# Optimization experiments

Measured on AMD Instinct MI355X. Metric: run time of the kernel, lower is better.

Reference implementation:

```python
import jax, jax.numpy as jnp
import numpy as np

B = 64          # batch
N_IN = 1_000_000  # SNPs (n_inputs)
N_OUT = 20_000    # genes (n_outputs = mask.shape[1])
KMAX = 64         # filter_size = max SNPs per gene


def setup_inputs() -> dict:
    key = jax.random.key(0)
    k1, k2, k3, k4 = jax.random.split(key, 4)
    x = jax.random.normal(k1, (B, N_IN), dtype=jnp.float32)
    kernel = jax.random.normal(k2, (KMAX, N_OUT), dtype=jnp.float32) * 0.05
    bias = jnp.zeros((N_OUT, 1), dtype=jnp.float32)
    # static COO mask encoded as padded per-gene index table + valid lengths
    gather_idx = jax.random.randint(k3, (N_OUT, KMAX), 0, N_IN, dtype=jnp.int32)
    lengths = jax.random.randint(k4, (N_OUT,), 1, KMAX + 1, dtype=jnp.int32)
    return {"x": x, "kernel": kernel, "bias": bias,
            "gather_idx": gather_idx, "lengths": lengths}


def reference(x, kernel, bias, gather_idx, lengths):
    # valid[g,k] = 1 if slot k of gene g holds a real SNP (padding mask)
    valid = (jnp.arange(KMAX, dtype=lengths.dtype)[None, :] < lengths[:, None])
    # per-gene weights, zeroed at padded slots: (G, K)
    w = jnp.where(valid, kernel.T, jnp.zeros((), dtype=kernel.dtype))
    # gather inputs per gene group: (B, G, K)
    gathered = x[:, gather_idx]
    # grouped multiply-reduce: (B, G)
    out = jnp.einsum('bgk,gk->bg', gathered, w)
    # bias per (gene, filter), filters = 1 -> output (B, G, 1)
    out = out[..., None] + bias[None, :, :]
    return out  # linear activation
```

## Files before the change

### kernel.cpp

```cpp
#include <hip/hip_runtime.h>
#include <hip/hip_bf16.h>

#define B_DIM 64
#define N_IN 1000000
#define N_OUT 20000
#define KMAX 64
#define GPB 16

__device__ __forceinline__ unsigned short f32_to_bf16_bits(float f) {
    __hip_bfloat16 b = __float2bfloat16(f);
    unsigned short s;
    __builtin_memcpy(&s, &b, sizeof(s));
    return s;
}

#define ZERO_BLOCKS 245
__global__ __launch_bounds__(256) void prep_kernel(
    uint4* __restrict__ flags4, const float* __restrict__ kern, float* __restrict__ wT) {
    if (blockIdx.x < ZERO_BLOCKS) {
        int tid = blockIdx.x * 256 + threadIdx.x;
        if (tid < N_IN / 16) flags4[tid] = uint4{0, 0, 0, 0};
        return;
    }
    __shared__ float lds[64 * 65];
    const int c0 = (blockIdx.x - ZERO_BLOCKS) * 64;
    const int t  = threadIdx.x;
    const int cq = t & 63;
    const int rq = t >> 6;
#pragma unroll
    for (int i = 0; i < 16; ++i) {
        int r = i * 4 + rq;
        int c = c0 + cq;
        if (c < N_OUT) lds[r * 65 + cq] = kern[r * N_OUT + c];
    }
    __syncthreads();
#pragma unroll
    for (int i = 0; i < 16; ++i) {
        int c = i * 4 + rq;
        int r = cq;
        if (c0 + c < N_OUT) wT[(c0 + c) * 64 + r] = lds[r * 65 + c];
    }
}

__global__ __launch_bounds__(256) void build_flags(
    const int* __restrict__ gidx, const int* __restrict__ lengths,
    unsigned char* __restrict__ flags) {
    int tid = blockIdx.x * 256 + threadIdx.x;
    int g = tid >> 6, k = tid & 63;
    if (g < N_OUT && k < lengths[g]) flags[gidx[g * KMAX + k]] = 1;
    if (tid == 0) flags[0] = 1;
}

__global__ __launch_bounds__(256) void transpose_x_bf16_masked(
    const float* __restrict__ src, __hip_bfloat16* __restrict__ dst,
    const unsigned char* __restrict__ flags) {
    __shared__ float ldsT[64 * 65];
    __shared__ unsigned char f[64];
    const int t  = threadIdx.x;
    const int c0 = blockIdx.x * 64;
    if (t < 64) f[t] = flags[c0 + t];
    const int col4 = (t & 15) * 4;
    const int r0   = t >> 4;
#pragma unroll
    for (int i = 0; i < 4; ++i) {
        int r = r0 + 16 * i;
        float4 v = *reinterpret_cast<const float4*>(&src[(size_t)r * N_IN + c0 + col4]);
        ldsT[(col4 + 0) * 65 + r] = v.x;
        ldsT[(col4 + 1) * 65 + r] = v.y;
        ldsT[(col4 + 2) * 65 + r] = v.z;
        ldsT[(col4 + 3) * 65 + r] = v.w;
    }
    __syncthreads();
    const int m = t & 15;
    const int cb = t >> 4;
#pragma unroll
    for (int i = 0; i < 4; ++i) {
        int c = cb + 16 * i;
        if (f[c]) {
            ushort4 h;
            h.x = f32_to_bf16_bits(ldsT[c * 65 + m * 4 + 0]);
            h.y = f32_to_bf16_bits(ldsT[c * 65 + m * 4 + 1]);
            h.z = f32_to_bf16_bits(ldsT[c * 65 + m * 4 + 2]);
            h.w = f32_to_bf16_bits(ldsT[c * 65 + m * 4 + 3]);
            *reinterpret_cast<ushort4*>(&dst[(size_t)(c0 + c) * 64 + m * 4]) = h;
        }
    }
}

__global__ __launch_bounds__(1024) void gather_dot_fused(
    const __hip_bfloat16* __restrict__ xT,
    const float* __restrict__ wT,
    const int*   __restrict__ gidx,
    const int*   __restrict__ lengths,
    const float* __restrict__ bias,
    float*       __restrict__ out) {
    __shared__ float sm[64 * 17];
    const int wave = threadIdx.x >> 6;
    const int lane = threadIdx.x & 63;
    const int half = lane >> 5;
    const int l    = lane & 31;
    const int g0   = blockIdx.x * GPB;
    const int g    = g0 + wave;

    const int len = lengths[g];
    const int   idx_l = (lane < len) ? gidx[g * KMAX + lane] : 0;
    const float w_l   = (lane < len) ? wT[g * KMAX + lane] : 0.0f;

    float acc0 = 0.0f, acc1 = 0.0f;
    for (int k = 0; k < len; k += 8) {
#pragma unroll
        for (int j = 0; j < 4; ++j) {
            int   kk  = k + 2 * j + half;
            int   row = __shfl(idx_l, kk);
            float w   = __shfl(w_l, kk);
            unsigned int u = *reinterpret_cast<const unsigned int*>(
                &xT[(size_t)row * 64 + 2 * l]);
            float f0 = __uint_as_float(u << 16);
            float f1 = __uint_as_float(u & 0xFFFF0000u);
            acc0 = fmaf(f0, w, acc0);
            acc1 = fmaf(f1, w, acc1);
        }
    }
    acc0 += __shfl_xor(acc0, 32);
    acc1 += __shfl_xor(acc1, 32);
    if (half == 0) {
        sm[(2 * l + 0) * 17 + wave] = acc0;
        sm[(2 * l + 1) * 17 + wave] = acc1;
    }
    __syncthreads();
    const int b = threadIdx.x >> 4;
    const int c = threadIdx.x & 15;
    out[(size_t)b * N_OUT + g0 + c] = sm[b * 17 + c] + bias[g0 + c];
}

__global__ __launch_bounds__(256) void direct_kernel(
    const float* __restrict__ x, const float* __restrict__ kern,
    const float* __restrict__ bias, const int* __restrict__ gidx,
    const int* __restrict__ lengths, float* __restrict__ out) {
    const int wave = threadIdx.x >> 6;
    const int lane = threadIdx.x & 63;
    const int g = blockIdx.x * 4 + wave;
    if (g >= N_OUT) return;
    const int len = lengths[g];
    float acc = 0.0f;
    for (int k = 0; k < len; ++k) {
        int   idx = gidx[g * KMAX + k];
        float w   = kern[k * N_OUT + g];
        acc = fmaf(x[(size_t)lane * N_IN + idx], w, acc);
    }
    out[(size_t)lane * N_OUT + g] = acc + bias[g];
}

extern "C" void kernel_launch(void* const* d_in, const int* in_sizes, int n_in,
                              void* d_out, int out_size, void* d_ws, size_t ws_size,
                              hipStream_t stream) {
    const float* x       = (const float*)d_in[0];
    const float* kern    = (const float*)d_in[1];
    const float* bias    = (const float*)d_in[2];
    const int*   gidx    = (const int*)d_in[3];
    const int*   lengths = (const int*)d_in[4];
    float*       out     = (float*)d_out;

    const size_t xT_bytes = (size_t)N_IN * B_DIM * sizeof(__hip_bfloat16);
    const size_t wT_bytes = (size_t)N_OUT * KMAX * sizeof(float);
    const size_t fl_bytes = (size_t)N_IN;

    if (ws_size >= xT_bytes + wT_bytes + fl_bytes) {
        __hip_bfloat16* xT    = (__hip_bfloat16*)d_ws;
        float*          wT    = (float*)((char*)d_ws + xT_bytes);
        unsigned char*  flags = (unsigned char*)((char*)d_ws + xT_bytes + wT_bytes);

        prep_kernel<<<ZERO_BLOCKS + (N_OUT + 63) / 64, 256, 0, stream>>>(
            (uint4*)flags, kern, wT);
        build_flags<<<N_OUT * KMAX / 256, 256, 0, stream>>>(gidx, lengths, flags);
        transpose_x_bf16_masked<<<N_IN / 64, 256, 0, stream>>>(x, xT, flags);
        gather_dot_fused<<<N_OUT / GPB, 1024, 0, stream>>>(xT, wT, gidx, lengths, bias, out);
    } else {
        direct_kernel<<<N_OUT / 4, 256, 0, stream>>>(x, kern, bias, gidx, lengths, out);
    }
}
```

Measured before the change: 91.47 us.

## Fuse flag build into prep, drop flag zeroing, widen packed-bf16 x transpose

Folds the flag-setting pass into the prep kernel, using int4 index loads, and removes the separate pass that zeroed the flag buffer. Setting a flag to a magic value still marks every needed row each call, so stale or garbage bytes can only cause extra rows to be written, never missing ones. The x transpose now handles 256 columns per 512-thread block. It packs two bf16 rows into one 32-bit word in LDS, which halves LDS traffic and gives wider stores, and a separate tail block covers the last 64 columns. The aim is fewer launches and more efficient transposition of the large x read, at the cost of more LDS per block and possible extra writes from uninitialized flag bytes.

```diff
diff --git a/kernel.cpp b/kernel.cpp
--- a/kernel.cpp
+++ b/kernel.cpp
@@ -6,6 +6,11 @@
 #define N_OUT 20000
 #define KMAX 64
 #define GPB 16
+#define COLS 256
+#define NFULL 3906
+#define TAILC 64
+#define FLAG_MAGIC 1
+#define FB 1250
 
 __device__ __forceinline__ unsigned short f32_to_bf16_bits(float f) {
     __hip_bfloat16 b = __float2bfloat16(f);
@@ -13,17 +18,29 @@
     __builtin_memcpy(&s, &b, sizeof(s));
     return s;
 }
-
-#define ZERO_BLOCKS 245
+__device__ __forceinline__ unsigned int pack_bf16x2(float lo, float hi) {
+    return (unsigned int)f32_to_bf16_bits(lo) | ((unsigned int)f32_to_bf16_bits(hi) << 16);
+}
+
 __global__ __launch_bounds__(256) void prep_kernel(
-    uint4* __restrict__ flags4, const float* __restrict__ kern, float* __restrict__ wT) {
-    if (blockIdx.x < ZERO_BLOCKS) {
+    const int* __restrict__ gidx, const int* __restrict__ lengths,
+    unsigned char* __restrict__ flags,
+    const float* __restrict__ kern, float* __restrict__ wT) {
+    if (blockIdx.x < FB) {
         int tid = blockIdx.x * 256 + threadIdx.x;
-        if (tid < N_IN / 16) flags4[tid] = uint4{0, 0, 0, 0};
+        int g  = tid >> 4;
+        int k4 = (tid & 15) * 4;
+        int len = lengths[g];
+        int4 v = *reinterpret_cast<const int4*>(&gidx[g * KMAX + k4]);
+        if (k4 + 0 < len) flags[v.x] = FLAG_MAGIC;
+        if (k4 + 1 < len) flags[v.y] = FLAG_MAGIC;
+        if (k4 + 2 < len) flags[v.z] = FLAG_MAGIC;
+        if (k4 + 3 < len) flags[v.w] = FLAG_MAGIC;
+        if (tid == 0) flags[0] = FLAG_MAGIC;
         return;
     }
     __shared__ float lds[64 * 65];
-    const int c0 = (blockIdx.x - ZERO_BLOCKS) * 64;
+    const int c0 = (blockIdx.x - FB) * 64;
     const int t  = threadIdx.x;
     const int cq = t & 63;
     const int rq = t >> 6;
@@ -42,47 +59,55 @@
     }
 }
 
-__global__ __launch_bounds__(256) void build_flags(
-    const int* __restrict__ gidx, const int* __restrict__ lengths,
-    unsigned char* __restrict__ flags) {
-    int tid = blockIdx.x * 256 + threadIdx.x;
-    int g = tid >> 6, k = tid & 63;
-    if (g < N_OUT && k < lengths[g]) flags[gidx[g * KMAX + k]] = 1;
-    if (tid == 0) flags[0] = 1;
-}
-
-__global__ __launch_bounds__(256) void transpose_x_bf16_masked(
+__global__ __launch_bounds__(512) void transpose_x(
     const float* __restrict__ src, __hip_bfloat16* __restrict__ dst,
     const unsigned char* __restrict__ flags) {
-    __shared__ float ldsT[64 * 65];
-    __shared__ unsigned char f[64];
+    __shared__ unsigned int lt32[COLS * 33];
+    __shared__ unsigned char f[COLS];
     const int t  = threadIdx.x;
-    const int c0 = blockIdx.x * 64;
-    if (t < 64) f[t] = flags[c0 + t];
-    const int col4 = (t & 15) * 4;
-    const int r0   = t >> 4;
-#pragma unroll
-    for (int i = 0; i < 4; ++i) {
-        int r = r0 + 16 * i;
-        float4 v = *reinterpret_cast<const float4*>(&src[(size_t)r * N_IN + c0 + col4]);
-        ldsT[(col4 + 0) * 65 + r] = v.x;
-        ldsT[(col4 + 1) * 65 + r] = v.y;
-        ldsT[(col4 + 2) * 65 + r] = v.z;
-        ldsT[(col4 + 3) * 65 + r] = v.w;
+    const bool full = blockIdx.x < NFULL;
+    const size_t c0 = (size_t)blockIdx.x * COLS;
+    const int CN = full ? COLS : TAILC;
+    if (t < CN) f[t] = flags[c0 + t];
+
+    if (full) {
+        const int w = t >> 6;
+        const int a = t & 63;
+#pragma unroll
+        for (int i = 0; i < 4; ++i) {
+            int r0 = i * 16 + w * 2;
+            float4 v0 = *reinterpret_cast<const float4*>(&src[(size_t)r0 * N_IN + c0 + a * 4]);
+            float4 v1 = *reinterpret_cast<const float4*>(&src[(size_t)(r0 + 1) * N_IN + c0 + a * 4]);
+            int c = a * 4, h = r0 >> 1;
+            lt32[(c + 0) * 33 + h] = pack_bf16x2(v0.x, v1.x);
+            lt32[(c + 1) * 33 + h] = pack_bf16x2(v0.y, v1.y);
+            lt32[(c + 2) * 33 + h] = pack_bf16x2(v0.z, v1.z);
+            lt32[(c + 3) * 33 + h] = pack_bf16x2(v0.w, v1.w);
+        }
+    } else {
+        if (t < 256) {
+            const int c = t & 63;
+            const int rp = t >> 6;
+#pragma unroll
+            for (int i = 0; i < 8; ++i) {
+                int r0 = i * 8 + rp * 2;
+                float x0 = src[(size_t)r0 * N_IN + c0 + c];
+                float x1 = src[(size_t)(r0 + 1) * N_IN + c0 + c];
+                lt32[c * 33 + (r0 >> 1)] = pack_bf16x2(x0, x1);
+            }
+        }
     }
     __syncthreads();
-    const int m = t & 15;
+    const int m  = t & 15;
     const int cb = t >> 4;
 #pragma unroll
-    for (int i = 0; i < 4; ++i) {
-        int c = cb + 16 * i;
-        if (f[c]) {
-            ushort4 h;
-            h.x = f32_to_bf16_bits(ldsT[c * 65 + m * 4 + 0]);
-            h.y = f32_to_bf16_bits(ldsT[c * 65 + m * 4 + 1]);
-            h.z = f32_to_bf16_bits(ldsT[c * 65 + m * 4 + 2]);
-            h.w = f32_to_bf16_bits(ldsT[c * 65 + m * 4 + 3]);
-            *reinterpret_cast<ushort4*>(&dst[(size_t)(c0 + c) * 64 + m * 4]) = h;
+    for (int i = 0; i < 8; ++i) {
+        int c = cb + 32 * i;
+        if (c < CN && f[c] == FLAG_MAGIC) {
+            uint2 u;
+            u.x = lt32[c * 33 + 2 * m];
+            u.y = lt32[c * 33 + 2 * m + 1];
+            *reinterpret_cast<uint2*>(&dst[(c0 + c) * 64 + m * 4]) = u;
         }
     }
 }
@@ -170,10 +195,9 @@
         float*          wT    = (float*)((char*)d_ws + xT_bytes);
         unsigned char*  flags = (unsigned char*)((char*)d_ws + xT_bytes + wT_bytes);
 
-        prep_kernel<<<ZERO_BLOCKS + (N_OUT + 63) / 64, 256, 0, stream>>>(
-            (uint4*)flags, kern, wT);
-        build_flags<<<N_OUT * KMAX / 256, 256, 0, stream>>>(gidx, lengths, flags);
-        transpose_x_bf16_masked<<<N_IN / 64, 256, 0, stream>>>(x, xT, flags);
+        prep_kernel<<<FB + (N_OUT + 63) / 64, 256, 0, stream>>>(
+            gidx, lengths, flags, kern, wT);
+        transpose_x<<<NFULL + 1, 512, 0, stream>>>(x, xT, flags);
         gather_dot_fused<<<N_OUT / GPB, 1024, 0, stream>>>(xT, wT, gidx, lengths, bias, out);
     } else {
         direct_kernel<<<N_OUT / 4, 256, 0, stream>>>(x, kern, bias, gidx, lengths, out);
```

Measured after the change: 90.18 us. No clear change (-1.4%).
